# Kernel tuning notes

Measured on AMD Instinct MI355X. Metric: run time of the kernel, lower is better.

The kernel has to match this reference:

```python
import jax, jax.numpy as jnp
import numpy as np

EMBED_DIM = 2048
NUM_HEADS = 16
HEAD_DIM = EMBED_DIM // NUM_HEADS


def setup_inputs() -> dict:
    key = jax.random.key(0)
    k_x, k_qkv, k_out = jax.random.split(key, 3)
    x = jax.random.normal(k_x, (4, 2048, EMBED_DIM), dtype=jnp.float32)
    # torch nn.Linear(in, out) weight is [out, in]; y = x @ W.T
    scale = 1.0 / np.sqrt(EMBED_DIM)
    W_qkv = jax.random.uniform(k_qkv, (3 * EMBED_DIM, EMBED_DIM), dtype=jnp.float32, minval=-scale, maxval=scale)
    W_out = jax.random.uniform(k_out, (EMBED_DIM, EMBED_DIM), dtype=jnp.float32, minval=-scale, maxval=scale)
    return {"x": x, "W_qkv": W_qkv, "W_out": W_out}


def reference(x, W_qkv, W_out):
    B, T, C = x.shape
    H, D = NUM_HEADS, HEAD_DIM
    qkv = jnp.einsum("btc,fc->btf", x, W_qkv)  # [B,T,3C]
    q, k, v = jnp.split(qkv, 3, axis=-1)
    q = q.reshape(B, T, H, D).transpose(0, 2, 1, 3)  # [B,H,T,D]
    k = k.reshape(B, T, H, D).transpose(0, 2, 1, 3)
    v = v.reshape(B, T, H, D).transpose(0, 2, 1, 3)
    att = jnp.einsum("bhqd,bhkd->bhqk", q, k) / jnp.sqrt(jnp.float32(D))
    causal = jnp.tril(jnp.ones((T, T), dtype=bool))
    att = jnp.where(causal[None, None], att, -jnp.inf)
    att = jax.nn.softmax(att, axis=-1)
    out = jnp.einsum("bhqk,bhkd->bhqd", att, v)  # [B,H,T,D]
    out = out.transpose(0, 2, 1, 3).reshape(B, T, C)
    return jnp.einsum("btc,oc->bto", out, W_out)
```

## Files before the change

kernel.cpp:

```cpp
#include <hip/hip_runtime.h>
#include <hip/hip_bf16.h>
#include <math.h>

#define BDIM 4
#define TDIM 2048
#define CDIM 2048
#define HDIM 16
#define DDIM 128
#define MROWS (BDIM*TDIM)
#define NQKV (3*CDIM)
#define GK   CDIM
#define QSZ  (MROWS*CDIM)

#define NTILES 32
#define NITER  16
#define HT     8192
#define BOFF   32768

typedef __attribute__((ext_vector_type(8))) short short8;
typedef __attribute__((ext_vector_type(4))) unsigned short ushort4v;
typedef __attribute__((ext_vector_type(4))) float f32x4;

__device__ __forceinline__ unsigned short f2bf(float f) {
    unsigned int u = __float_as_uint(f);
    u += 0x7fffu + ((u >> 16) & 1u);
    return (unsigned short)(u >> 16);
}

__device__ __forceinline__ void gload16(const unsigned short* g, unsigned short* l) {
    __builtin_amdgcn_global_load_lds((__attribute__((address_space(1))) void*)(g),
                                     (__attribute__((address_space(3))) void*)(l),
                                     16, 0, 0);
}

__global__ __launch_bounds__(256) void cvt_bf16(const float* __restrict__ in,
                                                unsigned short* __restrict__ outp,
                                                int n4)
{
    const int stride = gridDim.x * blockDim.x;
    for (int i = blockIdx.x * blockDim.x + threadIdx.x; i < n4; i += stride) {
        float4 f = ((const float4*)in)[i];
        ushort4v u;
        u[0] = f2bf(f.x); u[1] = f2bf(f.y); u[2] = f2bf(f.z); u[3] = f2bf(f.w);
        ((ushort4v*)outp)[i] = u;
    }
}

__device__ __forceinline__ void stage_half(const unsigned short* __restrict__ T,
                                           int rowbase, int kcol,
                                           unsigned short* dst, int w, int lane)
{
    const int sw = ((lane & 3) ^ ((lane >> 3) & 3)) * 8;
#pragma unroll
    for (int j = 0; j < 2; ++j) {
        const int r = w*32 + j*16 + (lane >> 2);
        gload16(T + (size_t)(rowbase + r)*GK + kcol + sw, dst + (w*32 + j*16)*32);
    }
}

template<int MQ, int KS, int BUF, bool RDB, bool WAIT>
__device__ __forceinline__ void gphase(unsigned short* lds,
    const unsigned short* __restrict__ stT, int stRow, int stKcol, unsigned short* stDst,
    int wr, int wc, int fr, int colu, int w, int lane,
    short8 (&bfr)[4], f32x4 (&acc)[8][4])
{
    const unsigned short* Ah = lds + (BUF*2 + KS)*HT;
    const unsigned short* Bh = lds + BOFF + (BUF*2 + KS)*HT;
    short8 af[4];
#pragma unroll
    for (int mi = 0; mi < 4; ++mi)
        af[mi] = *(const short8*)&Ah[(wr*128 + (MQ*4 + mi)*16 + fr)*32 + colu];
    if (RDB) {
#pragma unroll
        for (int nj = 0; nj < 4; ++nj)
            bfr[nj] = *(const short8*)&Bh[(wc*64 + nj*16 + fr)*32 + colu];
    }
    stage_half(stT, stRow, stKcol, stDst, w, lane);
    if (WAIT) asm volatile("s_waitcnt vmcnt(4)" ::: "memory");
    __builtin_amdgcn_s_barrier();
    asm volatile("s_waitcnt lgkmcnt(0)" ::: "memory");
    __builtin_amdgcn_sched_barrier(0);
    __builtin_amdgcn_s_setprio(1);
#pragma unroll
    for (int mi = 0; mi < 4; ++mi)
#pragma unroll
        for (int nj = 0; nj < 4; ++nj)
            acc[MQ*4 + mi][nj] = __builtin_amdgcn_mfma_f32_16x16x32_bf16(af[mi], bfr[nj], acc[MQ*4 + mi][nj], 0, 0, 0);
    __builtin_amdgcn_s_setprio(0);
    __builtin_amdgcn_s_barrier();
}

template<int MODE>
__global__ __launch_bounds__(512, 2) void gemm8(const unsigned short* __restrict__ A,
                                                const unsigned short* __restrict__ B,
                                                float* __restrict__ outp,
                                                unsigned short* __restrict__ qb,
                                                unsigned short* __restrict__ kb,
                                                unsigned short* __restrict__ vt,
                                                int Nsz)
{
    extern __shared__ unsigned short lds[];
    const int tid  = threadIdx.x;
    const int w    = tid >> 6;
    const int lane = tid & 63;
    const int wr   = w >> 2, wc = w & 3;
    const int fr   = lane & 15;
    const int fg   = lane >> 4;
    const int colu = (fg ^ ((fr >> 1) & 3)) * 8;
    const int m0   = blockIdx.x * 256, n0 = blockIdx.y * 256;

    f32x4 acc[8][4];
#pragma unroll
    for (int i = 0; i < 8; ++i)
#pragma unroll
        for (int j = 0; j < 4; ++j) acc[i][j] = (f32x4)(0.f);
    short8 bfr[4];

    stage_half(A, m0, 0,  lds,             w, lane);
    stage_half(B, n0, 0,  lds + BOFF,      w, lane);
    stage_half(A, m0, 32, lds + HT,        w, lane);
    stage_half(B, n0, 32, lds + BOFF + HT, w, lane);
    stage_half(A, m0, 64, lds + 2*HT,        w, lane);
    stage_half(B, n0, 64, lds + BOFF + 2*HT, w, lane);
    asm volatile("s_waitcnt vmcnt(0)" ::: "memory");
    __builtin_amdgcn_s_barrier();

    for (int i = 0; i < NITER; ++i) {
        const int t1 = 2*i + 1;
        const int t2 = (2*i + 2 < NTILES) ? 2*i + 2 : 0;
        const int t3 = (2*i + 3 < NTILES) ? 2*i + 3 : 0;
        gphase<0,0,0,true ,false>(lds, A, m0, t1*64+32, lds + 3*HT,        wr, wc, fr, colu, w, lane, bfr, acc);
        gphase<1,0,0,false,false>(lds, B, n0, t1*64+32, lds + BOFF + 3*HT, wr, wc, fr, colu, w, lane, bfr, acc);
        gphase<0,1,0,true ,false>(lds, A, m0, t2*64,    lds,               wr, wc, fr, colu, w, lane, bfr, acc);
        gphase<1,1,0,false,true >(lds, B, n0, t2*64,    lds + BOFF,        wr, wc, fr, colu, w, lane, bfr, acc);
        gphase<0,0,1,true ,false>(lds, A, m0, t2*64+32, lds + HT,          wr, wc, fr, colu, w, lane, bfr, acc);
        gphase<1,0,1,false,false>(lds, B, n0, t2*64+32, lds + BOFF + HT,   wr, wc, fr, colu, w, lane, bfr, acc);
        gphase<0,1,1,true ,false>(lds, A, m0, t3*64,    lds + 2*HT,        wr, wc, fr, colu, w, lane, bfr, acc);
        gphase<1,1,1,false,true >(lds, B, n0, t3*64,    lds + BOFF + 2*HT, wr, wc, fr, colu, w, lane, bfr, acc);
    }
    asm volatile("s_waitcnt vmcnt(0)" ::: "memory");

    if (MODE == 0) {
#pragma unroll
        for (int mi = 0; mi < 8; ++mi)
#pragma unroll
            for (int nj = 0; nj < 4; ++nj) {
                const int n   = n0 + wc*64 + nj*16 + fr;
                const int sel = n >> 11;
                const int c   = n & 2047;
                const int hh  = c >> 7, dd = c & 127;
                const int mb  = m0 + wr*128 + mi*16 + fg*4;
                const int bb  = mb >> 11, tt = mb & 2047;
                if (sel == 2) {
                    ushort4v v;
#pragma unroll
                    for (int r = 0; r < 4; ++r) v[r] = f2bf(acc[mi][nj][r]);
                    *(ushort4v*)&vt[((size_t)(bb*HDIM + hh)*DDIM + dd)*TDIM + tt] = v;
                } else {
                    unsigned short* dstb = (sel == 0) ? qb : kb;
#pragma unroll
                    for (int r = 0; r < 4; ++r)
                        dstb[((size_t)(bb*HDIM + hh)*TDIM + tt + r)*DDIM + dd] = f2bf(acc[mi][nj][r]);
                }
            }
    } else {
#pragma unroll
        for (int mi = 0; mi < 8; ++mi)
#pragma unroll
            for (int nj = 0; nj < 4; ++nj) {
                const int n = n0 + wc*64 + nj*16 + fr;
#pragma unroll
                for (int r = 0; r < 4; ++r) {
                    const int m = m0 + wr*128 + mi*16 + fg*4 + r;
                    outp[(size_t)m*Nsz + n] = acc[mi][nj][r];
                }
            }
    }
}

__global__ __launch_bounds__(256) void attn_mfma(const unsigned short* __restrict__ Qg,
                                                 const unsigned short* __restrict__ Kg,
                                                 const unsigned short* __restrict__ Vt,
                                                 unsigned short* __restrict__ attb)
{
    __shared__ __align__(16) unsigned short Ks[2][64*128];
    __shared__ __align__(16) unsigned short Vs[128*64];
    __shared__ __align__(16) unsigned short Ps[4*16*64];

    const int tid  = threadIdx.x;
    const int w    = tid >> 6;
    const int lane = tid & 63;
    const int g    = lane >> 4;
    const int c    = lane & 15;
    const int bh   = blockIdx.x & 63;
    const int qt   = 31 - (blockIdx.x >> 6);
    const int q0   = qt * 64;
    const float sc = 0.08838834764831845f;

    const unsigned short* Kbh  = Kg + (size_t)bh*TDIM*DDIM;
    const unsigned short* Vtbh = Vt + (size_t)bh*DDIM*TDIM;

    short8 qf[4];
    {
        const unsigned short* qrow = Qg + ((size_t)bh*TDIM + q0 + w*16 + c)*DDIM + g*8;
#pragma unroll
        for (int s = 0; s < 4; ++s)
            qf[s] = *(const short8*)(qrow + s*32);
    }

    f32x4 oacc[8];
#pragma unroll
    for (int i = 0; i < 8; ++i) oacc[i] = (f32x4)(0.f);
    float m_r[4], l_r[4];
#pragma unroll
    for (int r = 0; r < 4; ++r) { m_r[r] = -INFINITY; l_r[r] = 0.f; }

#define STAGE_K(buf, kt_)                                                        \
    {                                                                            \
        _Pragma("unroll")                                                        \
        for (int j = 0; j < 4; ++j) {                                            \
            const int rw  = w*16 + j*4 + (lane >> 4);                            \
            const int sub = (lane & 15) ^ (rw & 7);                              \
            gload16(Kbh + ((size_t)((kt_)*64 + rw))*DDIM + sub*8,                \
                    &Ks[buf][w*2048 + j*512]);                                   \
        }                                                                        \
    }
#define STAGE_V(kt_)                                                             \
    {                                                                            \
        _Pragma("unroll")                                                        \
        for (int j = 0; j < 4; ++j) {                                            \
            const int d   = w*32 + j*8 + (lane >> 3);                            \
            const int sub = (lane & 7) ^ (d & 7);                                \
            gload16(Vtbh + (size_t)d*TDIM + (kt_)*64 + sub*8,                    \
                    &Vs[w*2048 + j*512]);                                        \
        }                                                                        \
    }

    STAGE_K(0, 0);
    STAGE_V(0);
    __syncthreads();

    for (int kt = 0; kt <= qt; ++kt) {
        const int cur = kt & 1;
        if (kt < qt) STAGE_K(cur ^ 1, kt + 1);
        if (kt > 0)  STAGE_V(kt);

        f32x4 sa[4];
#pragma unroll
        for (int n = 0; n < 4; ++n) sa[n] = (f32x4)(0.f);
#pragma unroll
        for (int s = 0; s < 4; ++s)
#pragma unroll
            for (int n = 0; n < 4; ++n) {
                const int row = n*16 + c;
                short8 bf = *(const short8*)&Ks[cur][(row*128 + s*32 + g*8) ^ ((row&7)<<3)];
                sa[n] = __builtin_amdgcn_mfma_f32_16x16x32_bf16(qf[s], bf, sa[n], 0, 0, 0);
            }

        if (kt == qt) {
#pragma unroll
            for (int n = 0; n < 4; ++n) {
                const int k = n*16 + c;
#pragma unroll
                for (int r = 0; r < 4; ++r) {
                    const int q = w*16 + g*4 + r;
                    if (k > q) sa[n][r] = -INFINITY;
                }
            }
        }

        float corr[4];
#pragma unroll
        for (int r = 0; r < 4; ++r) {
            float mx = fmaxf(fmaxf(sa[0][r], sa[1][r]), fmaxf(sa[2][r], sa[3][r]));
            mx = fmaxf(mx, __shfl_xor(mx, 1));
            mx = fmaxf(mx, __shfl_xor(mx, 2));
            mx = fmaxf(mx, __shfl_xor(mx, 4));
            mx = fmaxf(mx, __shfl_xor(mx, 8));
            const float mn = fmaxf(m_r[r], mx);
            corr[r] = __expf((m_r[r] - mn) * sc);
            float rs = 0.f;
#pragma unroll
            for (int n = 0; n < 4; ++n) {
                const float p = __expf((sa[n][r] - mn) * sc);
                sa[n][r] = p;
                rs += p;
            }
            rs += __shfl_xor(rs, 1);
            rs += __shfl_xor(rs, 2);
            rs += __shfl_xor(rs, 4);
            rs += __shfl_xor(rs, 8);
            l_r[r] = l_r[r]*corr[r] + rs;
            m_r[r] = mn;
        }
#pragma unroll
        for (int i = 0; i < 8; ++i) {
            f32x4 o = oacc[i];
            o[0] *= corr[0]; o[1] *= corr[1]; o[2] *= corr[2]; o[3] *= corr[3];
            oacc[i] = o;
        }

        unsigned short* Pw = &Ps[w*1024];
#pragma unroll
        for (int n = 0; n < 4; ++n)
#pragma unroll
            for (int r = 0; r < 4; ++r) {
                const int q = g*4 + r, k = n*16 + c;
                Pw[(q*64 + k) ^ ((q&7)<<3)] = f2bf(sa[n][r]);
            }
        short8 pf[2];
#pragma unroll
        for (int s2 = 0; s2 < 2; ++s2)
            pf[s2] = *(const short8*)&Pw[(c*64 + s2*32 + g*8) ^ ((c&7)<<3)];

        __syncthreads();

#pragma unroll
        for (int s2 = 0; s2 < 2; ++s2)
#pragma unroll
            for (int dt = 0; dt < 8; ++dt) {
                const int d = dt*16 + c;
                short8 vf = *(const short8*)&Vs[(d*64 + s2*32 + g*8) ^ ((d&7)<<3)];
                oacc[dt] = __builtin_amdgcn_mfma_f32_16x16x32_bf16(pf[s2], vf, oacc[dt], 0, 0, 0);
            }

        __syncthreads();
    }

    float inv[4];
#pragma unroll
    for (int r = 0; r < 4; ++r) inv[r] = 1.f / l_r[r];
    const int b = bh >> 4, h = bh & 15;
    unsigned short* obase = attb + ((size_t)b*TDIM + q0 + w*16 + g*4)*CDIM + h*DDIM + c;
#pragma unroll
    for (int dt = 0; dt < 8; ++dt)
#pragma unroll
        for (int r = 0; r < 4; ++r)
            obase[(size_t)r*CDIM + dt*16] = f2bf(oacc[dt][r] * inv[r]);
}

extern "C" void kernel_launch(void* const* d_in, const int* in_sizes, int n_in,
                              void* d_out, int out_size, void* d_ws, size_t ws_size,
                              hipStream_t stream)
{
    const float* x    = (const float*)d_in[0];
    const float* Wqkv = (const float*)d_in[1];
    const float* Wout = (const float*)d_in[2];
    float* out = (float*)d_out;

    unsigned short* ws = (unsigned short*)d_ws;
    unsigned short* xb    = ws;
    unsigned short* Wqkvb = xb    + (size_t)MROWS*CDIM;
    unsigned short* Woutb = Wqkvb + (size_t)NQKV*CDIM;
    unsigned short* Qb    = Woutb + (size_t)CDIM*CDIM;
    unsigned short* Kb    = Qb + QSZ;
    unsigned short* Vtb   = Kb + QSZ;
    unsigned short* attb  = Vtb + QSZ;

    cvt_bf16<<<2048, 256, 0, stream>>>(x,    xb,    MROWS*CDIM/4);
    cvt_bf16<<<2048, 256, 0, stream>>>(Wqkv, Wqkvb, NQKV*CDIM/4);
    cvt_bf16<<<1024, 256, 0, stream>>>(Wout, Woutb, CDIM*CDIM/4);
    gemm8<0><<<dim3(MROWS/256, NQKV/256), 512, 131072, stream>>>(xb, Wqkvb, nullptr, Qb, Kb, Vtb, NQKV);
    attn_mfma<<<dim3(64*32), 256, 0, stream>>>(Qb, Kb, Vtb, attb);
    gemm8<1><<<dim3(MROWS/256, CDIM/256), 512, 131072, stream>>>(attb, Woutb, out, nullptr, nullptr, nullptr, CDIM);
}
```

Measured before the change: 460.1 us.

## Enlarge attention query tile to 128 rows with 8 waves and prescaled Q

The attention kernel now processes 128 query rows per block using 512 threads (8 waves), so each staged K/V tile is shared by twice as many waves. The grid is halved, and dynamic shared memory of 64 KB is requested. The softmax scale times log2(e) is folded into Q at the QKV GEMM epilogue, so the kernel can use exp2f directly. Waves whose rows lie entirely before the current key tile skip their compute, but they still take part in the barriers. This adds idle waves on the diagonal tiles and raises LDS use per block, which may lower occupancy.

Result: no change. 461.7 us (+0.3%).

```diff
diff --git a/kernel.cpp b/kernel.cpp
--- a/kernel.cpp
+++ b/kernel.cpp
@@ -16,6 +16,8 @@
 #define NITER  16
 #define HT     8192
 #define BOFF   32768
+
+#define QSCALE 0.1275171f
 
 typedef __attribute__((ext_vector_type(8))) short short8;
 typedef __attribute__((ext_vector_type(4))) unsigned short ushort4v;
@@ -156,11 +158,14 @@
 #pragma unroll
                     for (int r = 0; r < 4; ++r) v[r] = f2bf(acc[mi][nj][r]);
                     *(ushort4v*)&vt[((size_t)(bb*HDIM + hh)*DDIM + dd)*TDIM + tt] = v;
+                } else if (sel == 0) {
+#pragma unroll
+                    for (int r = 0; r < 4; ++r)
+                        qb[((size_t)(bb*HDIM + hh)*TDIM + tt + r)*DDIM + dd] = f2bf(acc[mi][nj][r] * QSCALE);
                 } else {
-                    unsigned short* dstb = (sel == 0) ? qb : kb;
 #pragma unroll
                     for (int r = 0; r < 4; ++r)
-                        dstb[((size_t)(bb*HDIM + hh)*TDIM + tt + r)*DDIM + dd] = f2bf(acc[mi][nj][r]);
+                        kb[((size_t)(bb*HDIM + hh)*TDIM + tt + r)*DDIM + dd] = f2bf(acc[mi][nj][r]);
                 }
             }
     } else {
@@ -178,14 +183,15 @@
     }
 }
 
-__global__ __launch_bounds__(256) void attn_mfma(const unsigned short* __restrict__ Qg,
+__global__ __launch_bounds__(512) void attn_mfma(const unsigned short* __restrict__ Qg,
                                                  const unsigned short* __restrict__ Kg,
                                                  const unsigned short* __restrict__ Vt,
                                                  unsigned short* __restrict__ attb)
 {
-    __shared__ __align__(16) unsigned short Ks[2][64*128];
-    __shared__ __align__(16) unsigned short Vs[128*64];
-    __shared__ __align__(16) unsigned short Ps[4*16*64];
+    extern __shared__ unsigned short smem[];
+    unsigned short* KsB = smem;
+    unsigned short* Vs  = smem + 16384;
+    unsigned short* Ps  = smem + 24576;
 
     const int tid  = threadIdx.x;
     const int w    = tid >> 6;
@@ -193,16 +199,17 @@
     const int g    = lane >> 4;
     const int c    = lane & 15;
     const int bh   = blockIdx.x & 63;
-    const int qt   = 31 - (blockIdx.x >> 6);
-    const int q0   = qt * 64;
-    const float sc = 0.08838834764831845f;
+    const int qb_  = 15 - (blockIdx.x >> 6);
+    const int q0   = qb_ * 128;
+    const int qt   = 2*qb_ + 1;
+    const int qw   = q0 + w*16;
 
     const unsigned short* Kbh  = Kg + (size_t)bh*TDIM*DDIM;
     const unsigned short* Vtbh = Vt + (size_t)bh*DDIM*TDIM;
 
     short8 qf[4];
     {
-        const unsigned short* qrow = Qg + ((size_t)bh*TDIM + q0 + w*16 + c)*DDIM + g*8;
+        const unsigned short* qrow = Qg + ((size_t)bh*TDIM + qw + c)*DDIM + g*8;
 #pragma unroll
         for (int s = 0; s < 4; ++s)
             qf[s] = *(const short8*)(qrow + s*32);
@@ -218,21 +225,21 @@
 #define STAGE_K(buf, kt_)                                                        \
     {                                                                            \
         _Pragma("unroll")                                                        \
-        for (int j = 0; j < 4; ++j) {                                            \
-            const int rw  = w*16 + j*4 + (lane >> 4);                            \
+        for (int j = 0; j < 2; ++j) {                                            \
+            const int rw  = (w<<3) + (j<<2) + (lane >> 4);                       \
             const int sub = (lane & 15) ^ (rw & 7);                              \
             gload16(Kbh + ((size_t)((kt_)*64 + rw))*DDIM + sub*8,                \
-                    &Ks[buf][w*2048 + j*512]);                                   \
+                    &KsB[(buf)*8192 + ((w<<3) + (j<<2))*128]);                   \
         }                                                                        \
     }
 #define STAGE_V(kt_)                                                             \
     {                                                                            \
         _Pragma("unroll")                                                        \
-        for (int j = 0; j < 4; ++j) {                                            \
-            const int d   = w*32 + j*8 + (lane >> 3);                            \
+        for (int j = 0; j < 2; ++j) {                                            \
+            const int d   = (w<<4) + (j<<3) + (lane >> 3);                       \
             const int sub = (lane & 7) ^ (d & 7);                                \
             gload16(Vtbh + (size_t)d*TDIM + (kt_)*64 + sub*8,                    \
-                    &Vs[w*2048 + j*512]);                                        \
+                    &Vs[((w<<4) + (j<<3))*64]);                                  \
         }                                                                        \
     }
 
@@ -245,84 +252,90 @@
         if (kt < qt) STAGE_K(cur ^ 1, kt + 1);
         if (kt > 0)  STAGE_V(kt);
 
-        f32x4 sa[4];
-#pragma unroll
-        for (int n = 0; n < 4; ++n) sa[n] = (f32x4)(0.f);
-#pragma unroll
-        for (int s = 0; s < 4; ++s)
-#pragma unroll
-            for (int n = 0; n < 4; ++n) {
-                const int row = n*16 + c;
-                short8 bf = *(const short8*)&Ks[cur][(row*128 + s*32 + g*8) ^ ((row&7)<<3)];
-                sa[n] = __builtin_amdgcn_mfma_f32_16x16x32_bf16(qf[s], bf, sa[n], 0, 0, 0);
-            }
-
-        if (kt == qt) {
-#pragma unroll
-            for (int n = 0; n < 4; ++n) {
-                const int k = n*16 + c;
+        const bool active = (kt*64) <= (qw + 15);
+        short8 pf[2];
+
+        if (active) {
+            f32x4 sa[4];
+#pragma unroll
+            for (int n = 0; n < 4; ++n) sa[n] = (f32x4)(0.f);
+#pragma unroll
+            for (int s = 0; s < 4; ++s)
+#pragma unroll
+                for (int n = 0; n < 4; ++n) {
+                    const int row = n*16 + c;
+                    short8 bf = *(const short8*)&KsB[cur*8192 + ((row*128 + s*32 + g*8) ^ ((row&7)<<3))];
+                    sa[n] = __builtin_amdgcn_mfma_f32_16x16x32_bf16(qf[s], bf, sa[n], 0, 0, 0);
+                }
+
+            if (kt*64 + 63 > qw) {
+#pragma unroll
+                for (int n = 0; n < 4; ++n) {
+                    const int kgl = kt*64 + n*16 + c;
+#pragma unroll
+                    for (int r = 0; r < 4; ++r) {
+                        const int qgl = qw + g*4 + r;
+                        if (kgl > qgl) sa[n][r] = -INFINITY;
+                    }
+                }
+            }
+
+            float corr[4];
+#pragma unroll
+            for (int r = 0; r < 4; ++r) {
+                float mx = fmaxf(fmaxf(sa[0][r], sa[1][r]), fmaxf(sa[2][r], sa[3][r]));
+                mx = fmaxf(mx, __shfl_xor(mx, 1));
+                mx = fmaxf(mx, __shfl_xor(mx, 2));
+                mx = fmaxf(mx, __shfl_xor(mx, 4));
+                mx = fmaxf(mx, __shfl_xor(mx, 8));
+                const float mn = fmaxf(m_r[r], mx);
+                corr[r] = exp2f(m_r[r] - mn);
+                float rs = 0.f;
+#pragma unroll
+                for (int n = 0; n < 4; ++n) {
+                    const float p = exp2f(sa[n][r] - mn);
+                    sa[n][r] = p;
+                    rs += p;
+                }
+                rs += __shfl_xor(rs, 1);
+                rs += __shfl_xor(rs, 2);
+                rs += __shfl_xor(rs, 4);
+                rs += __shfl_xor(rs, 8);
+                l_r[r] = l_r[r]*corr[r] + rs;
+                m_r[r] = mn;
+            }
+#pragma unroll
+            for (int i = 0; i < 8; ++i) {
+                f32x4 o = oacc[i];
+                o[0] *= corr[0]; o[1] *= corr[1]; o[2] *= corr[2]; o[3] *= corr[3];
+                oacc[i] = o;
+            }
+
+            unsigned short* Pw = &Ps[w*1024];
+#pragma unroll
+            for (int n = 0; n < 4; ++n)
 #pragma unroll
                 for (int r = 0; r < 4; ++r) {
-                    const int q = w*16 + g*4 + r;
-                    if (k > q) sa[n][r] = -INFINITY;
-                }
-            }
+                    const int q = g*4 + r, k = n*16 + c;
+                    Pw[(q*64 + k) ^ ((q&7)<<3)] = f2bf(sa[n][r]);
+                }
+#pragma unroll
+            for (int s2 = 0; s2 < 2; ++s2)
+                pf[s2] = *(const short8*)&Pw[(c*64 + s2*32 + g*8) ^ ((c&7)<<3)];
         }
 
-        float corr[4];
-#pragma unroll
-        for (int r = 0; r < 4; ++r) {
-            float mx = fmaxf(fmaxf(sa[0][r], sa[1][r]), fmaxf(sa[2][r], sa[3][r]));
-            mx = fmaxf(mx, __shfl_xor(mx, 1));
-            mx = fmaxf(mx, __shfl_xor(mx, 2));
-            mx = fmaxf(mx, __shfl_xor(mx, 4));
-            mx = fmaxf(mx, __shfl_xor(mx, 8));
-            const float mn = fmaxf(m_r[r], mx);
-            corr[r] = __expf((m_r[r] - mn) * sc);
-            float rs = 0.f;
-#pragma unroll
-            for (int n = 0; n < 4; ++n) {
-                const float p = __expf((sa[n][r] - mn) * sc);
-                sa[n][r] = p;
-                rs += p;
-            }
-            rs += __shfl_xor(rs, 1);
-            rs += __shfl_xor(rs, 2);
-            rs += __shfl_xor(rs, 4);
-            rs += __shfl_xor(rs, 8);
-            l_r[r] = l_r[r]*corr[r] + rs;
-            m_r[r] = mn;
+        __syncthreads();
+
+        if (active) {
+#pragma unroll
+            for (int s2 = 0; s2 < 2; ++s2)
+#pragma unroll
+                for (int dt = 0; dt < 8; ++dt) {
+                    const int d = dt*16 + c;
+                    short8 vf = *(const short8*)&Vs[(d*64 + s2*32 + g*8) ^ ((d&7)<<3)];
+                    oacc[dt] = __builtin_amdgcn_mfma_f32_16x16x32_bf16(pf[s2], vf, oacc[dt], 0, 0, 0);
+                }
         }
-#pragma unroll
-        for (int i = 0; i < 8; ++i) {
-            f32x4 o = oacc[i];
-            o[0] *= corr[0]; o[1] *= corr[1]; o[2] *= corr[2]; o[3] *= corr[3];
-            oacc[i] = o;
-        }
-
-        unsigned short* Pw = &Ps[w*1024];
-#pragma unroll
-        for (int n = 0; n < 4; ++n)
-#pragma unroll
-            for (int r = 0; r < 4; ++r) {
-                const int q = g*4 + r, k = n*16 + c;
-                Pw[(q*64 + k) ^ ((q&7)<<3)] = f2bf(sa[n][r]);
-            }
-        short8 pf[2];
-#pragma unroll
-        for (int s2 = 0; s2 < 2; ++s2)
-            pf[s2] = *(const short8*)&Pw[(c*64 + s2*32 + g*8) ^ ((c&7)<<3)];
-
-        __syncthreads();
-
-#pragma unroll
-        for (int s2 = 0; s2 < 2; ++s2)
-#pragma unroll
-            for (int dt = 0; dt < 8; ++dt) {
-                const int d = dt*16 + c;
-                short8 vf = *(const short8*)&Vs[(d*64 + s2*32 + g*8) ^ ((d&7)<<3)];
-                oacc[dt] = __builtin_amdgcn_mfma_f32_16x16x32_bf16(pf[s2], vf, oacc[dt], 0, 0, 0);
-            }
 
         __syncthreads();
     }
@@ -331,7 +344,7 @@
 #pragma unroll
     for (int r = 0; r < 4; ++r) inv[r] = 1.f / l_r[r];
     const int b = bh >> 4, h = bh & 15;
-    unsigned short* obase = attb + ((size_t)b*TDIM + q0 + w*16 + g*4)*CDIM + h*DDIM + c;
+    unsigned short* obase = attb + ((size_t)b*TDIM + qw + g*4)*CDIM + h*DDIM + c;
 #pragma unroll
     for (int dt = 0; dt < 8; ++dt)
 #pragma unroll
@@ -361,6 +374,6 @@
     cvt_bf16<<<2048, 256, 0, stream>>>(Wqkv, Wqkvb, NQKV*CDIM/4);
     cvt_bf16<<<1024, 256, 0, stream>>>(Wout, Woutb, CDIM*CDIM/4);
     gemm8<0><<<dim3(MROWS/256, NQKV/256), 512, 131072, stream>>>(xb, Wqkvb, nullptr, Qb, Kb, Vtb, NQKV);
-    attn_mfma<<<dim3(64*32), 256, 0, stream>>>(Qb, Kb, Vtb, attb);
+    attn_mfma<<<dim3(64*16), 512, 65536, stream>>>(Qb, Kb, Vtb, attb);
     gemm8<1><<<dim3(MROWS/256, CDIM/256), 512, 131072, stream>>>(attb, Woutb, out, nullptr, nullptr, nullptr, CDIM);
 }
```
